# Kernel tuning notes

Hardware: AMD Instinct MI355X
Metric: run time of the kernel (lower is better)

## Reference

```python
import jax, jax.numpy as jnp
import numpy as np

N = 100000
E = 1600000
D = 64
R = 200


def setup_inputs() -> dict:
    key = jax.random.key(0)
    k = jax.random.split(key, 7)
    return {
        "h": jax.random.normal(k[0], (N, D), dtype=jnp.float32),
        "e": jax.random.normal(k[1], (E, D), dtype=jnp.float32),
        "weight": jax.random.normal(k[2], (R, D), dtype=jnp.float32),
        "attention": jax.random.normal(k[3], (R, D), dtype=jnp.float32),
        "src": jax.random.randint(k[4], (E,), 0, N, dtype=jnp.int32),
        "dst": jax.random.randint(k[5], (E,), 0, N, dtype=jnp.int32),
        "rel": jax.random.randint(k[6], (E,), 0, R, dtype=jnp.int32),
    }


def reference(h, e, weight, attention, src, dst, rel):
    # msg_func: per-edge relation-indexed gather + elementwise mul-add
    # msg[k] = h[src[k]] * weight[rel[k]] + e[k] * attention[rel[k]]
    msg = h[src] * weight[rel] + e * attention[rel]  # [E, D]
    # reduce_func: h_new = h + sum of incoming messages (segment-sum over dst)
    agg = jax.ops.segment_sum(msg, dst, num_segments=N)  # [N, D]
    return h + agg
```

## Files before the change

kernel.cpp:

```cpp
#include <hip/hip_runtime.h>

#define DIM 64
#define SCAN_BLOCK 256
#define ELEMS_PER_THREAD 8
#define ELEMS_PER_BLOCK (SCAN_BLOCK * ELEMS_PER_THREAD)


__global__ void hist_kernel(const int* __restrict__ dst, int* __restrict__ counts, int E) {
    int k = blockIdx.x * blockDim.x + threadIdx.x;
    if (k < E) atomicAdd(&counts[dst[k]], 1);
}

__global__ void scan1_kernel(const int* __restrict__ counts, int* __restrict__ offsets,
                             int* __restrict__ bsums, int N) {
    __shared__ int lds[SCAN_BLOCK];
    int base = blockIdx.x * ELEMS_PER_BLOCK + threadIdx.x * ELEMS_PER_THREAD;
    int v[ELEMS_PER_THREAD];
    int tsum = 0;
#pragma unroll
    for (int i = 0; i < ELEMS_PER_THREAD; ++i) {
        int idx = base + i;
        v[i] = (idx < N) ? counts[idx] : 0;
        tsum += v[i];
    }
    lds[threadIdx.x] = tsum;
    __syncthreads();
    for (int off = 1; off < SCAN_BLOCK; off <<= 1) {
        int t = (threadIdx.x >= off) ? lds[threadIdx.x - off] : 0;
        __syncthreads();
        lds[threadIdx.x] += t;
        __syncthreads();
    }
    int incl = lds[threadIdx.x];
    int running = incl - tsum;
#pragma unroll
    for (int i = 0; i < ELEMS_PER_THREAD; ++i) {
        int idx = base + i;
        if (idx < N) offsets[idx] = running;
        running += v[i];
    }
    if (threadIdx.x == SCAN_BLOCK - 1) bsums[blockIdx.x] = incl;
}

__global__ void scan2_kernel(int* __restrict__ bsums, int nb) {
    if (blockIdx.x == 0 && threadIdx.x == 0) {
        int run = 0;
        for (int i = 0; i < nb; ++i) { int c = bsums[i]; bsums[i] = run; run += c; }
    }
}

__global__ void scan3_kernel(int* __restrict__ offsets, int* __restrict__ cursor,
                             const int* __restrict__ bsums, int N, int E) {
    int i = blockIdx.x * blockDim.x + threadIdx.x;
    if (i < N) {
        int o = offsets[i] + bsums[i / ELEMS_PER_BLOCK];
        offsets[i] = o;
        cursor[i] = o;
    }
    if (i == 0) offsets[N] = E;
}

__global__ void scatter_kernel(const int* __restrict__ dst, int* __restrict__ cursor,
                               int* __restrict__ perm, int E) {
    int k = blockIdx.x * blockDim.x + threadIdx.x;
    if (k < E) {
        int p = atomicAdd(&cursor[dst[k]], 1);
        perm[p] = k;
    }
}


__global__ void gather_kernel(const float* __restrict__ h, const float* __restrict__ e,
                              const float* __restrict__ w, const float* __restrict__ att,
                              const int* __restrict__ src, const int* __restrict__ rel,
                              const int* __restrict__ offsets, const int* __restrict__ perm,
                              float* __restrict__ out, int N) {
    int wave = (int)(((long long)blockIdx.x * blockDim.x + threadIdx.x) >> 6);
    int lane = threadIdx.x & 63;
    if (wave >= N) return;

    int start = offsets[wave];
    int end   = offsets[wave + 1];
    float acc = h[(size_t)wave * DIM + lane];

    for (int b = start; b < end; b += 64) {
        int cnt = min(64, end - b);
        int kk = 0, ss = 0, rr = 0;
        if (lane < cnt) {
            kk = perm[b + lane];
            ss = src[kk];
            rr = rel[kk];
        }
        for (int j = 0; j < cnt; ++j) {
            int k = __shfl(kk, j);
            int s = __shfl(ss, j);
            int r = __shfl(rr, j);
            acc += h[(size_t)s * DIM + lane] * w[(size_t)r * DIM + lane]
                 + e[(size_t)k * DIM + lane] * att[(size_t)r * DIM + lane];
        }
    }
    out[(size_t)wave * DIM + lane] = acc;
}


__global__ void init_out_kernel(const float* __restrict__ h, float* __restrict__ out, int n4) {
    int i = blockIdx.x * blockDim.x + threadIdx.x;
    if (i < n4)
        reinterpret_cast<float4*>(out)[i] = reinterpret_cast<const float4*>(h)[i];
}

__global__ void edge_msg_kernel(const float* __restrict__ h, const float* __restrict__ e,
                                const float* __restrict__ w, const float* __restrict__ att,
                                const int* __restrict__ src, const int* __restrict__ dst,
                                const int* __restrict__ rel, float* __restrict__ out, int E) {
    long long tid = (long long)blockIdx.x * blockDim.x + threadIdx.x;
    int k = (int)(tid >> 4);
    if (k >= E) return;
    int q = ((int)tid & 15) << 2;
    int s = src[k], d = dst[k], r = rel[k];
    const float4 hv  = *reinterpret_cast<const float4*>(h   + (size_t)s * DIM + q);
    const float4 ev  = *reinterpret_cast<const float4*>(e   + (size_t)k * DIM + q);
    const float4 wv  = *reinterpret_cast<const float4*>(w   + (size_t)r * DIM + q);
    const float4 av  = *reinterpret_cast<const float4*>(att + (size_t)r * DIM + q);
    float4 m;
    m.x = hv.x * wv.x + ev.x * av.x;
    m.y = hv.y * wv.y + ev.y * av.y;
    m.z = hv.z * wv.z + ev.z * av.z;
    m.w = hv.w * wv.w + ev.w * av.w;
    float* o = out + (size_t)d * DIM + q;
    atomicAdd(o + 0, m.x);
    atomicAdd(o + 1, m.y);
    atomicAdd(o + 2, m.z);
    atomicAdd(o + 3, m.w);
}

extern "C" void kernel_launch(void* const* d_in, const int* in_sizes, int n_in,
                              void* d_out, int out_size, void* d_ws, size_t ws_size,
                              hipStream_t stream) {
    const float* h   = (const float*)d_in[0];
    const float* e   = (const float*)d_in[1];
    const float* w   = (const float*)d_in[2];
    const float* att = (const float*)d_in[3];
    const int* src   = (const int*)d_in[4];
    const int* dst   = (const int*)d_in[5];
    const int* rel   = (const int*)d_in[6];
    float* out       = (float*)d_out;

    const int N = in_sizes[0] / DIM;
    const int E = in_sizes[1] / DIM;

    const int nb = (N + ELEMS_PER_BLOCK - 1) / ELEMS_PER_BLOCK;
    const int nb_pad = (nb + 63) & ~63;

    size_t need = ((size_t)3 * N + 1 + nb_pad + E) * sizeof(int);

    if (ws_size < need) {
        int n4 = N * (DIM / 4);
        init_out_kernel<<<(n4 + 255) / 256, 256, 0, stream>>>(h, out, n4);
        long long total = (long long)E * 16;
        int blocks = (int)((total + 255) / 256);
        edge_msg_kernel<<<blocks, 256, 0, stream>>>(h, e, w, att, src, dst, rel, out, E);
        return;
    }

    int* counts  = (int*)d_ws;
    int* offsets = counts + N;
    int* cursor  = offsets + N + 1;
    int* bsums   = cursor + N;
    int* perm    = bsums + nb_pad;

    hipMemsetAsync(counts, 0, (size_t)N * sizeof(int), stream);

    hist_kernel<<<(E + 255) / 256, 256, 0, stream>>>(dst, counts, E);
    scan1_kernel<<<nb, SCAN_BLOCK, 0, stream>>>(counts, offsets, bsums, N);
    scan2_kernel<<<1, 64, 0, stream>>>(bsums, nb);
    scan3_kernel<<<(N + 255) / 256, 256, 0, stream>>>(offsets, cursor, bsums, N, E);
    scatter_kernel<<<(E + 255) / 256, 256, 0, stream>>>(dst, cursor, perm, E);

    long long threads = (long long)N * 64;
    int gblocks = (int)((threads + 255) / 256);
    gather_kernel<<<gblocks, 256, 0, stream>>>(h, e, w, att, src, rel, offsets, perm, out, N);
}
```

Measured before the change: 861.0 us.

## Pack edge id, src, rel into CSR entries and unroll gather by four

The scatter pass now writes an int4 (edge id, src, rel) per CSR slot, so the gather no longer does dependent loads of src and rel through the permutation. The inner gather loop is unrolled by four to issue more independent row loads per wave, which helps hide latency. The single-thread block-sum scan becomes a wave-wide shuffle scan, and the counts buffer is reused as cursor to save workspace. The trade is extra scatter writes of 16 bytes per edge, which raises workspace traffic.

Result: faster. 796.1 us (-7.5%).

```diff
diff --git a/kernel.cpp b/kernel.cpp
--- a/kernel.cpp
+++ b/kernel.cpp
@@ -43,9 +43,18 @@
 }
 
 __global__ void scan2_kernel(int* __restrict__ bsums, int nb) {
-    if (blockIdx.x == 0 && threadIdx.x == 0) {
-        int run = 0;
-        for (int i = 0; i < nb; ++i) { int c = bsums[i]; bsums[i] = run; run += c; }
+    int lane = threadIdx.x;
+    int carry = 0;
+    for (int base = 0; base < nb; base += 64) {
+        int i = base + lane;
+        int orig = (i < nb) ? bsums[i] : 0;
+        int v = orig;
+        for (int off = 1; off < 64; off <<= 1) {
+            int t = __shfl_up(v, off);
+            if (lane >= off) v += t;
+        }
+        if (i < nb) bsums[i] = carry + v - orig;
+        carry += __shfl(v, 63);
     }
 }
 
@@ -60,20 +69,20 @@
     if (i == 0) offsets[N] = E;
 }
 
-__global__ void scatter_kernel(const int* __restrict__ dst, int* __restrict__ cursor,
-                               int* __restrict__ perm, int E) {
+__global__ void scatter_kernel(const int* __restrict__ dst, const int* __restrict__ src,
+                               const int* __restrict__ rel, int* __restrict__ cursor,
+                               int4* __restrict__ perm4, int E) {
     int k = blockIdx.x * blockDim.x + threadIdx.x;
     if (k < E) {
         int p = atomicAdd(&cursor[dst[k]], 1);
-        perm[p] = k;
+        perm4[p] = make_int4(k, src[k], rel[k], 0);
     }
 }
 
 
 __global__ void gather_kernel(const float* __restrict__ h, const float* __restrict__ e,
                               const float* __restrict__ w, const float* __restrict__ att,
-                              const int* __restrict__ src, const int* __restrict__ rel,
-                              const int* __restrict__ offsets, const int* __restrict__ perm,
+                              const int* __restrict__ offsets, const int4* __restrict__ perm4,
                               float* __restrict__ out, int N) {
     int wave = (int)(((long long)blockIdx.x * blockDim.x + threadIdx.x) >> 6);
     int lane = threadIdx.x & 63;
@@ -85,16 +94,32 @@
 
     for (int b = start; b < end; b += 64) {
         int cnt = min(64, end - b);
-        int kk = 0, ss = 0, rr = 0;
-        if (lane < cnt) {
-            kk = perm[b + lane];
-            ss = src[kk];
-            rr = rel[kk];
+        int4 ent = make_int4(0, 0, 0, 0);
+        if (lane < cnt) ent = perm4[b + lane];
+
+        int j = 0;
+        for (; j + 4 <= cnt; j += 4) {
+            int k0 = __shfl(ent.x, j + 0), s0 = __shfl(ent.y, j + 0), r0 = __shfl(ent.z, j + 0);
+            int k1 = __shfl(ent.x, j + 1), s1 = __shfl(ent.y, j + 1), r1 = __shfl(ent.z, j + 1);
+            int k2 = __shfl(ent.x, j + 2), s2 = __shfl(ent.y, j + 2), r2 = __shfl(ent.z, j + 2);
+            int k3 = __shfl(ent.x, j + 3), s3 = __shfl(ent.y, j + 3), r3 = __shfl(ent.z, j + 3);
+
+            float e0 = e[(size_t)k0 * DIM + lane], h0 = h[(size_t)s0 * DIM + lane];
+            float w0 = w[(size_t)r0 * DIM + lane], a0 = att[(size_t)r0 * DIM + lane];
+            float e1 = e[(size_t)k1 * DIM + lane], h1 = h[(size_t)s1 * DIM + lane];
+            float w1 = w[(size_t)r1 * DIM + lane], a1 = att[(size_t)r1 * DIM + lane];
+            float e2 = e[(size_t)k2 * DIM + lane], h2 = h[(size_t)s2 * DIM + lane];
+            float w2 = w[(size_t)r2 * DIM + lane], a2 = att[(size_t)r2 * DIM + lane];
+            float e3 = e[(size_t)k3 * DIM + lane], h3 = h[(size_t)s3 * DIM + lane];
+            float w3 = w[(size_t)r3 * DIM + lane], a3 = att[(size_t)r3 * DIM + lane];
+
+            acc += h0 * w0 + e0 * a0;
+            acc += h1 * w1 + e1 * a1;
+            acc += h2 * w2 + e2 * a2;
+            acc += h3 * w3 + e3 * a3;
         }
-        for (int j = 0; j < cnt; ++j) {
-            int k = __shfl(kk, j);
-            int s = __shfl(ss, j);
-            int r = __shfl(rr, j);
+        for (; j < cnt; ++j) {
+            int k = __shfl(ent.x, j), s = __shfl(ent.y, j), r = __shfl(ent.z, j);
             acc += h[(size_t)s * DIM + lane] * w[(size_t)r * DIM + lane]
                  + e[(size_t)k * DIM + lane] * att[(size_t)r * DIM + lane];
         }
@@ -152,7 +177,7 @@
     const int nb = (N + ELEMS_PER_BLOCK - 1) / ELEMS_PER_BLOCK;
     const int nb_pad = (nb + 63) & ~63;
 
-    size_t need = ((size_t)3 * N + 1 + nb_pad + E) * sizeof(int);
+    size_t need = (size_t)E * 16 + ((size_t)2 * N + 1 + nb_pad) * sizeof(int);
 
     if (ws_size < need) {
         int n4 = N * (DIM / 4);
@@ -163,21 +188,20 @@
         return;
     }
 
-    int* counts  = (int*)d_ws;
-    int* offsets = counts + N;
+    int4* perm4  = (int4*)d_ws;
+    int* offsets = (int*)(perm4 + E);
     int* cursor  = offsets + N + 1;
     int* bsums   = cursor + N;
-    int* perm    = bsums + nb_pad;
-
-    hipMemsetAsync(counts, 0, (size_t)N * sizeof(int), stream);
-
-    hist_kernel<<<(E + 255) / 256, 256, 0, stream>>>(dst, counts, E);
-    scan1_kernel<<<nb, SCAN_BLOCK, 0, stream>>>(counts, offsets, bsums, N);
+
+    hipMemsetAsync(cursor, 0, (size_t)N * sizeof(int), stream);
+
+    hist_kernel<<<(E + 255) / 256, 256, 0, stream>>>(dst, cursor, E);
+    scan1_kernel<<<nb, SCAN_BLOCK, 0, stream>>>(cursor, offsets, bsums, N);
     scan2_kernel<<<1, 64, 0, stream>>>(bsums, nb);
     scan3_kernel<<<(N + 255) / 256, 256, 0, stream>>>(offsets, cursor, bsums, N, E);
-    scatter_kernel<<<(E + 255) / 256, 256, 0, stream>>>(dst, cursor, perm, E);
+    scatter_kernel<<<(E + 255) / 256, 256, 0, stream>>>(dst, src, rel, cursor, perm4, E);
 
     long long threads = (long long)N * 64;
     int gblocks = (int)((threads + 255) / 256);
-    gather_kernel<<<gblocks, 256, 0, stream>>>(h, e, w, att, src, rel, offsets, perm, out, N);
-}
+    gather_kernel<<<gblocks, 256, 0, stream>>>(h, e, w, att, offsets, perm4, out, N);
+}
```
